# Kernel tuning notes

Hardware: AMD Instinct MI355X
Metric: run time of the kernel (lower is better)

The kernel has to match this reference:

```python
import jax, jax.numpy as jnp
import numpy as np

# fixed geometry: N = B2D * H * W pixels
B2D, H, W = 32, 112, 112
NCLS, NSUB, DIM = 4, 2, 256
PROTO_MOM = 0.999
SK_ITERS, SK_EPS = 3, 0.05
LN_EPS = 1e-5


def layer_norm(x, gamma, beta):
    mu = jnp.mean(x, axis=-1, keepdims=True)
    var = jnp.var(x, axis=-1, keepdims=True)
    return (x - mu) * jax.lax.rsqrt(var + LN_EPS) * gamma + beta


def l2_normalize(x):
    return x / jnp.maximum(jnp.linalg.norm(x, axis=-1, keepdims=True), 1e-12)


def masked_sinkhorn(sim_c, mask):
    # sim_c: [N, M] cosine sims for one class; mask: [N] bool (pixels of this class)
    # Faithful to distributed_sinkhorn, restricted to masked rows.
    m = mask.astype(sim_c.dtype)
    L = jnp.exp(sim_c / SK_EPS).T * m[None, :]          # [M, N]
    Bn = jnp.sum(m)
    M = L.shape[0]
    L = L / jnp.maximum(jnp.sum(L), 1e-30)
    for _ in range(SK_ITERS):
        L = L / jnp.maximum(jnp.sum(L, axis=1, keepdims=True), 1e-30) / M
        col = jnp.sum(L, axis=0, keepdims=True)
        L = jnp.where(m[None, :] > 0, L / jnp.maximum(col, 1e-30) / jnp.maximum(Bn, 1.0), 0.0)
    L = (L * Bn).T                                       # [N, M]
    idx = jnp.argmax(L, axis=1)
    q = jax.nn.one_hot(idx, M, dtype=sim_c.dtype) * m[:, None]  # hard assignment
    return q, idx


def setup_inputs() -> dict:
    key = jax.random.key(0)
    ks = jax.random.split(key, 3)
    N = B2D * H * W
    return {
        "out_feat": jax.random.normal(ks[0], (N, DIM), dtype=jnp.float32),
        "label": jax.random.randint(ks[1], (N,), 0, NCLS, dtype=jnp.int64),
        "prototypes": jax.random.normal(ks[2], (NCLS, NSUB, DIM), dtype=jnp.float32),
        "fn_gamma": jnp.ones((DIM,), jnp.float32),
        "fn_beta": jnp.zeros((DIM,), jnp.float32),
        "mn_gamma": jnp.ones((NCLS,), jnp.float32),
        "mn_beta": jnp.zeros((NCLS,), jnp.float32),
    }


def reference(out_feat, label, prototypes, fn_gamma, fn_beta, mn_gamma, mn_beta):
    N = out_feat.shape[0]
    feat = l2_normalize(layer_norm(out_feat, fn_gamma, fn_beta))      # [N, D]
    protos = l2_normalize(prototypes)                                  # [K, M, D]
    sim = jnp.einsum('nd,kmd->nmk', feat, protos)                      # [N, M, K]
    nearest = layer_norm(jnp.max(sim, axis=1), mn_gamma, mn_beta)      # [N, K]
    pred = jnp.argmax(nearest, axis=-1)
    correct = (label == pred)                                          # [N] bool

    proto_logits = sim.reshape(N, NSUB * NCLS)
    proto_target = jnp.zeros((N,), jnp.float32)
    new_protos = protos
    for c in range(NCLS):
        cls_mask = (label == c)
        q, idx = masked_sinkhorn(sim[:, :, c], cls_mask)               # q:[N,M], masked
        mk = (cls_mask & correct).astype(feat.dtype)[:, None]
        m_q = q * mk                                                   # [N, M]
        f = m_q.T @ (feat * mk)                                        # [M, D]
        n = jnp.sum(m_q, axis=0)                                       # [M]
        f = l2_normalize(f)
        upd = PROTO_MOM * protos[c] + (1.0 - PROTO_MOM) * f
        upd = jnp.where(((jnp.sum(n) > 0) & (n != 0))[:, None], upd, protos[c])
        new_protos = new_protos.at[c].set(upd)
        proto_target = jnp.where(cls_mask, idx.astype(jnp.float32) + NSUB * c, proto_target)
    new_protos = l2_normalize(new_protos)

    nearest_img = nearest.reshape(B2D, H, W, NCLS).transpose(0, 3, 1, 2)  # [b, K, h, w]
    return nearest_img, proto_logits, proto_target, new_protos
```

## Files before the change

kernel.cpp:

```cpp
#include <hip/hip_runtime.h>
#include <stdint.h>

#define N_PIX 401408
#define HWIMG 12544
#define LN_EPS 1e-5f

struct Ws {
  double R[3][8];
  unsigned cnt4[4];
  unsigned nmk[8];
  float  protoN[8][256];
  float  fAcc[8][256];
  unsigned char flags[N_PIX];
};

__device__ __forceinline__ float wredf(float v) {
#pragma unroll
  for (int o = 32; o > 0; o >>= 1) v += __shfl_xor(v, o, 64);
  return v;
}
__device__ __forceinline__ float wred16(float v) {
  v += __shfl_xor(v, 1, 64);
  v += __shfl_xor(v, 2, 64);
  v += __shfl_xor(v, 4, 64);
  v += __shfl_xor(v, 8, 64);
  return v;
}
__device__ __forceinline__ double wredd(double v) {
#pragma unroll
  for (int o = 32; o > 0; o >>= 1) v += __shfl_xor(v, o, 64);
  return v;
}
__device__ __forceinline__ unsigned wredu(unsigned v) {
#pragma unroll
  for (int o = 32; o > 0; o >>= 1) v += (unsigned)__shfl_xor((int)v, o, 64);
  return v;
}

__global__ __launch_bounds__(256) void k_main(
    const float* __restrict__ X, const int* __restrict__ label,
    const float* __restrict__ protos,
    const float* __restrict__ fng, const float* __restrict__ fnb,
    const float* __restrict__ mng, const float* __restrict__ mnb,
    Ws* __restrict__ ws,
    float* __restrict__ out_nearest, float* __restrict__ out_logits) {
  __shared__ float prS[16 * 132];
  int tid = threadIdx.x;
  int wave = tid >> 6, lane = tid & 63;

  if (blockIdx.x == 0) {
    if (tid < 24) ((double*)ws->R)[tid] = 0.0;
    if (tid >= 24 && tid < 32) ws->nmk[tid - 24] = 0u;
    if (tid >= 32 && tid < 36) ws->cnt4[tid - 32] = 0u;
    for (int i = tid; i < 2048; i += 256) (&ws->fAcc[0][0])[i] = 0.f;
  }

#pragma unroll
  for (int t = 0; t < 2; t++) {
    int r = wave + t * 4;
    const float4 p = *(const float4*)(protos + r * 256 + lane * 4);
    float ss = p.x * p.x + p.y * p.y + p.z * p.z + p.w * p.w;
    ss = wredf(ss);
    float inv = 1.0f / fmaxf(sqrtf(ss), 1e-12f);
    float4 o; o.x = p.x * inv; o.y = p.y * inv; o.z = p.z * inv; o.w = p.w * inv;
    int sd = lane >> 2;
    *(float4*)(&prS[sd * 132 + r * 16 + (lane & 3) * 4]) = o;
    if (blockIdx.x == 0) *(float4*)(&ws->protoN[r][lane * 4]) = o;
  }
  __syncthreads();

  int grp = lane >> 4, s = lane & 15;
  int n = blockIdx.x * 16 + wave * 4 + grp;

  const float* xb = X + (size_t)n * 256 + s * 16;
  const float4 x0 = *(const float4*)(xb);
  const float4 x1 = *(const float4*)(xb + 4);
  const float4 x2 = *(const float4*)(xb + 8);
  const float4 x3 = *(const float4*)(xb + 12);
  int lab = label[n];

  float sm = (x0.x + x0.y + x0.z + x0.w) + (x1.x + x1.y + x1.z + x1.w) +
             (x2.x + x2.y + x2.z + x2.w) + (x3.x + x3.y + x3.z + x3.w);
  float q = x0.x * x0.x + x0.y * x0.y + x0.z * x0.z + x0.w * x0.w +
            x1.x * x1.x + x1.y * x1.y + x1.z * x1.z + x1.w * x1.w +
            x2.x * x2.x + x2.y * x2.y + x2.z * x2.z + x2.w * x2.w +
            x3.x * x3.x + x3.y * x3.y + x3.z * x3.z + x3.w * x3.w;
  sm = wred16(sm); q = wred16(q);
  float mu = sm * (1.0f / 256.0f);
  float var = q * (1.0f / 256.0f) - mu * mu;
  float rstd = rsqrtf(var + LN_EPS);

  const float* gb = fng + s * 16;
  const float* bb = fnb + s * 16;
  const float4 g0 = *(const float4*)(gb);
  const float4 g1 = *(const float4*)(gb + 4);
  const float4 g2 = *(const float4*)(gb + 8);
  const float4 g3 = *(const float4*)(gb + 12);
  const float4 b0 = *(const float4*)(bb);
  const float4 b1 = *(const float4*)(bb + 4);
  const float4 b2 = *(const float4*)(bb + 8);
  const float4 b3 = *(const float4*)(bb + 12);

  float4 y0, y1, y2, y3;
  y0.x = (x0.x - mu) * rstd * g0.x + b0.x; y0.y = (x0.y - mu) * rstd * g0.y + b0.y;
  y0.z = (x0.z - mu) * rstd * g0.z + b0.z; y0.w = (x0.w - mu) * rstd * g0.w + b0.w;
  y1.x = (x1.x - mu) * rstd * g1.x + b1.x; y1.y = (x1.y - mu) * rstd * g1.y + b1.y;
  y1.z = (x1.z - mu) * rstd * g1.z + b1.z; y1.w = (x1.w - mu) * rstd * g1.w + b1.w;
  y2.x = (x2.x - mu) * rstd * g2.x + b2.x; y2.y = (x2.y - mu) * rstd * g2.y + b2.y;
  y2.z = (x2.z - mu) * rstd * g2.z + b2.z; y2.w = (x2.w - mu) * rstd * g2.w + b2.w;
  y3.x = (x3.x - mu) * rstd * g3.x + b3.x; y3.y = (x3.y - mu) * rstd * g3.y + b3.y;
  y3.z = (x3.z - mu) * rstd * g3.z + b3.z; y3.w = (x3.w - mu) * rstd * g3.w + b3.w;

  float qq = y0.x * y0.x + y0.y * y0.y + y0.z * y0.z + y0.w * y0.w +
             y1.x * y1.x + y1.y * y1.y + y1.z * y1.z + y1.w * y1.w +
             y2.x * y2.x + y2.y * y2.y + y2.z * y2.z + y2.w * y2.w +
             y3.x * y3.x + y3.y * y3.y + y3.z * y3.z + y3.w * y3.w;
  qq = wred16(qq);

  float dot[8];
#pragma unroll
  for (int j = 0; j < 8; j++) {
    const float* pj = &prS[s * 132 + j * 16];
    const float4 pa = *(const float4*)(pj);
    const float4 pb = *(const float4*)(pj + 4);
    const float4 pc = *(const float4*)(pj + 8);
    const float4 pd = *(const float4*)(pj + 12);
    dot[j] = y0.x * pa.x + y0.y * pa.y + y0.z * pa.z + y0.w * pa.w +
             y1.x * pb.x + y1.y * pb.y + y1.z * pb.z + y1.w * pb.w +
             y2.x * pc.x + y2.y * pc.y + y2.z * pc.z + y2.w * pc.w +
             y3.x * pd.x + y3.y * pd.y + y3.z * pd.z + y3.w * pd.w;
  }
#pragma unroll
  for (int o = 1; o <= 4; o <<= 1) {
#pragma unroll
    for (int j = 0; j < 8; j++) dot[j] += __shfl_xor(dot[j], o, 64);
  }
  int bsel = s & 7;
  float t0 = (bsel & 1) ? dot[1] : dot[0];
  float t1 = (bsel & 1) ? dot[3] : dot[2];
  float t2 = (bsel & 1) ? dot[5] : dot[4];
  float t3 = (bsel & 1) ? dot[7] : dot[6];
  float u0 = (bsel & 2) ? t1 : t0;
  float u1v = (bsel & 2) ? t3 : t2;
  float v = (bsel & 4) ? u1v : u0;
  v += __shfl_xor(v, 8, 64);

  float inv = 1.0f / fmaxf(sqrtf(qq), 1e-12f);
  float d = v * inv;

  if (s < 8) out_logits[(size_t)n * 8 + ((s & 1) << 2) + (s >> 1)] = d;

  float nm = fmaxf(d, __shfl_xor(d, 1, 64));
  float tA = __shfl_xor(nm, 2, 64);
  float s2 = nm + tA, q2 = nm * nm + tA * tA;
  float s4 = s2 + __shfl_xor(s2, 4, 64);
  float q4 = q2 + __shfl_xor(q2, 4, 64);
  float m4 = 0.25f * s4;
  float v4 = 0.25f * q4 - m4 * m4;
  float rs4 = rsqrtf(v4 + LN_EPS);
  int k = (s >> 1) & 3;
  float lnv = (nm - m4) * rs4 * mng[k] + mnb[k];

  int bimg = n / HWIMG;
  int p = n - bimg * HWIMG;
  if (s < 8 && (s & 1) == 0)
    out_nearest[((size_t)bimg * 4 + k) * HWIMG + p] = lnv;

  float av = lnv; int ak = k;
#pragma unroll
  for (int o = 2; o <= 4; o <<= 1) {
    float ov = __shfl_xor(av, o, 64);
    int ok = __shfl_xor(ak, o, 64);
    bool take = (ov > av) || (ov == av && ok < ak);
    av = take ? ov : av;
    ak = take ? ok : ak;
  }
  if (s == 0) ws->flags[n] = (lab == ak) ? (unsigned char)1 : (unsigned char)0;
}

template <int ITER>
__global__ __launch_bounds__(256) void k_sink(const float* __restrict__ logits,
                                              const int* __restrict__ label,
                                              Ws* __restrict__ ws) {
  __shared__ float su1[8], su2[8], sBn[4];
  int tid = threadIdx.x;
  if (ITER >= 2) {
    if (tid < 8) {
      int c = tid >> 1;
      float S = (float)ws->R[0][c * 2] + (float)ws->R[0][c * 2 + 1];
      float uu0 = 1.0f / fmaxf(S, 1e-30f);
      float R0 = (float)ws->R[0][tid];
      float uu1 = uu0 / (fmaxf(uu0 * R0, 1e-30f) * 2.0f);
      su1[tid] = uu1;
      if (ITER >= 3) {
        float R1 = (float)ws->R[1][tid];
        su2[tid] = uu1 / (fmaxf(uu1 * R1, 1e-30f) * 2.0f);
      }
    }
    if (tid < 4) sBn[tid] = fmaxf((float)ws->cnt4[tid], 1.0f);
  }
  __syncthreads();

  double a0 = 0, a1 = 0, a2 = 0, a3 = 0, a4 = 0, a5 = 0, a6 = 0, a7 = 0;
  unsigned c0 = 0, c1 = 0, c2 = 0, c3 = 0;
  int gtid = blockIdx.x * 256 + tid;
  int T = gridDim.x * 256;
  for (int n = gtid; n < N_PIX; n += T) {
    int c = label[n];
    const float4 la = *(const float4*)(logits + (size_t)n * 8);
    const float4 lb = *(const float4*)(logits + (size_t)n * 8 + 4);
    float s0 = (c & 2) ? ((c & 1) ? la.w : la.z) : ((c & 1) ? la.y : la.x);
    float s1 = (c & 2) ? ((c & 1) ? lb.w : lb.z) : ((c & 1) ? lb.y : lb.x);
    float E0 = expf(s0 / 0.05f);
    float E1 = expf(s1 / 0.05f);
    float v = 1.0f;
    if (ITER >= 2) {
      float S1 = su1[c * 2] * E0 + su1[c * 2 + 1] * E1;
      float v1 = 1.0f / (fmaxf(S1, 1e-30f) * sBn[c]);
      v = v1;
      if (ITER >= 3) {
        float S2 = su2[c * 2] * E0 + su2[c * 2 + 1] * E1;
        v = v1 / (fmaxf(v1 * S2, 1e-30f) * sBn[c]);
      }
    }
    double t0 = (double)(v * E0), t1 = (double)(v * E1);
    if (c == 0) { a0 += t0; a1 += t1; c0++; }
    else if (c == 1) { a2 += t0; a3 += t1; c1++; }
    else if (c == 2) { a4 += t0; a5 += t1; c2++; }
    else { a6 += t0; a7 += t1; c3++; }
  }
  a0 = wredd(a0); a1 = wredd(a1); a2 = wredd(a2); a3 = wredd(a3);
  a4 = wredd(a4); a5 = wredd(a5); a6 = wredd(a6); a7 = wredd(a7);
  __shared__ double lds[4][8];
  __shared__ unsigned ldc[4][4];
  int wave = tid >> 6, lane = tid & 63;
  if (ITER == 1) { c0 = wredu(c0); c1 = wredu(c1); c2 = wredu(c2); c3 = wredu(c3); }
  if (lane == 0) {
    lds[wave][0] = a0; lds[wave][1] = a1; lds[wave][2] = a2; lds[wave][3] = a3;
    lds[wave][4] = a4; lds[wave][5] = a5; lds[wave][6] = a6; lds[wave][7] = a7;
    if (ITER == 1) { ldc[wave][0] = c0; ldc[wave][1] = c1; ldc[wave][2] = c2; ldc[wave][3] = c3; }
  }
  __syncthreads();
  if (tid < 8) {
    double ssum = lds[0][tid] + lds[1][tid] + lds[2][tid] + lds[3][tid];
    unsafeAtomicAdd(&ws->R[ITER - 1][tid], ssum);
  }
  if (ITER == 1 && tid < 4) {
    unsigned cs = ldc[0][tid] + ldc[1][tid] + ldc[2][tid] + ldc[3][tid];
    atomicAdd(&ws->cnt4[tid], cs);
  }
}

__global__ __launch_bounds__(256) void k_accum(
    const float* __restrict__ X, const int* __restrict__ label,
    const float* __restrict__ fng, const float* __restrict__ fnb,
    const float* __restrict__ logits, Ws* __restrict__ ws,
    float* __restrict__ out_target) {
  __shared__ float fa[4 * 2048];
  __shared__ float su[8];
  __shared__ unsigned ldc[4][8];
  int tid = threadIdx.x;
  if (tid < 8) {
    int c = tid >> 1;
    float S = (float)ws->R[0][c * 2] + (float)ws->R[0][c * 2 + 1];
    float uu0 = 1.0f / fmaxf(S, 1e-30f);
    float R0 = (float)ws->R[0][tid];
    float uu1 = uu0 / (fmaxf(uu0 * R0, 1e-30f) * 2.0f);
    float R1 = (float)ws->R[1][tid];
    float uu2 = uu1 / (fmaxf(uu1 * R1, 1e-30f) * 2.0f);
    float R2 = (float)ws->R[2][tid];
    su[tid] = uu2 / (fmaxf(uu2 * R2, 1e-30f) * 2.0f);
  }
  for (int i = tid; i < 4 * 2048; i += 256) fa[i] = 0.f;
  __syncthreads();

  int wave = tid >> 6, lane = tid & 63;
  const float4 g4 = *(const float4*)(fng + lane * 4);
  const float4 b4 = *(const float4*)(fnb + lane * 4);
  float* myAcc = &fa[wave * 2048];

  unsigned cl[8] = {0, 0, 0, 0, 0, 0, 0, 0};
  int gw = blockIdx.x * 4 + wave;
  int GW = gridDim.x * 4;
  for (int ch = gw; ch < N_PIX / 64; ch += GW) {
    int n = ch * 64 + lane;
    int c = label[n];
    int fl = ws->flags[n];
    float s0 = logits[(size_t)n * 8 + c];
    float s1 = logits[(size_t)n * 8 + 4 + c];
    float E0 = expf(s0 / 0.05f);
    float E1 = expf(s1 / 0.05f);
    int idx = (su[c * 2 + 1] * E1 > su[c * 2] * E0) ? 1 : 0;
    out_target[n] = (float)(idx + 2 * c);
    int bucket = c * 2 + idx;
#pragma unroll
    for (int j = 0; j < 8; j++) cl[j] += (fl && bucket == j) ? 1u : 0u;

    unsigned long long mask = __ballot(fl);
    while (mask) {
      int src = __builtin_ctzll(mask);
      mask &= (mask - 1);
      int cc = __shfl(c, src, 64);
      int ii = __shfl(idx, src, 64);
      int nn = ch * 64 + src;
      const float4 x = *(const float4*)(X + (size_t)nn * 256 + lane * 4);
      float s = x.x + x.y + x.z + x.w;
      float q = x.x * x.x + x.y * x.y + x.z * x.z + x.w * x.w;
      s = wredf(s); q = wredf(q);
      float mu = s * (1.0f / 256.0f);
      float var = q * (1.0f / 256.0f) - mu * mu;
      float rstd = rsqrtf(var + LN_EPS);
      float y0 = (x.x - mu) * rstd * g4.x + b4.x;
      float y1 = (x.y - mu) * rstd * g4.y + b4.y;
      float y2 = (x.z - mu) * rstd * g4.z + b4.z;
      float y3 = (x.w - mu) * rstd * g4.w + b4.w;
      float qq = y0 * y0 + y1 * y1 + y2 * y2 + y3 * y3;
      qq = wredf(qq);
      float inv = 1.0f / fmaxf(sqrtf(qq), 1e-12f);
      float* dst = myAcc + (cc * 2 + ii) * 256 + lane * 4;
      dst[0] += y0 * inv; dst[1] += y1 * inv; dst[2] += y2 * inv; dst[3] += y3 * inv;
    }
  }
#pragma unroll
  for (int j = 0; j < 8; j++) cl[j] = wredu(cl[j]);
  if (lane == 0) {
#pragma unroll
    for (int j = 0; j < 8; j++) ldc[wave][j] = cl[j];
  }
  __syncthreads();
  float* fg = &ws->fAcc[0][0];
  for (int i = tid; i < 2048; i += 256) {
    float ssum = fa[i] + fa[2048 + i] + fa[4096 + i] + fa[6144 + i];
    unsafeAtomicAdd(fg + i, ssum);
  }
  if (tid < 8) {
    unsigned cs = ldc[0][tid] + ldc[1][tid] + ldc[2][tid] + ldc[3][tid];
    if (cs) atomicAdd(&ws->nmk[tid], cs);
  }
}

__global__ __launch_bounds__(512) void k_final(Ws* __restrict__ ws, float* __restrict__ out_protos) {
  int tid = threadIdx.x;
  int r = tid >> 6, lane = tid & 63;
  const float4 f = *(const float4*)(&ws->fAcc[r][lane * 4]);
  float ss = wredf(f.x * f.x + f.y * f.y + f.z * f.z + f.w * f.w);
  float invf = 1.0f / fmaxf(sqrtf(ss), 1e-12f);
  unsigned nr = ws->nmk[r];
  int c = r >> 1;
  unsigned tot = ws->nmk[c * 2] + ws->nmk[c * 2 + 1];
  bool cond = (tot > 0u) && (nr != 0u);
  const float4 p = *(const float4*)(&ws->protoN[r][lane * 4]);
  float u0 = cond ? 0.999f * p.x + 0.001f * (f.x * invf) : p.x;
  float u1 = cond ? 0.999f * p.y + 0.001f * (f.y * invf) : p.y;
  float u2 = cond ? 0.999f * p.z + 0.001f * (f.z * invf) : p.z;
  float u3 = cond ? 0.999f * p.w + 0.001f * (f.w * invf) : p.w;
  float ss2 = wredf(u0 * u0 + u1 * u1 + u2 * u2 + u3 * u3);
  float invn = 1.0f / fmaxf(sqrtf(ss2), 1e-12f);
  float4 o; o.x = u0 * invn; o.y = u1 * invn; o.z = u2 * invn; o.w = u3 * invn;
  *(float4*)(out_protos + r * 256 + lane * 4) = o;
}

extern "C" void kernel_launch(void* const* d_in, const int* in_sizes, int n_in,
                              void* d_out, int out_size, void* d_ws, size_t ws_size,
                              hipStream_t stream) {
  const float* X = (const float*)d_in[0];
  const int* label = (const int*)d_in[1];
  const float* protos = (const float*)d_in[2];
  const float* fng = (const float*)d_in[3];
  const float* fnb = (const float*)d_in[4];
  const float* mng = (const float*)d_in[5];
  const float* mnb = (const float*)d_in[6];

  float* out = (float*)d_out;
  float* out_nearest = out;
  float* out_logits = out + 1605632;
  float* out_target = out_logits + 3211264;
  float* out_protos = out_target + N_PIX;
  Ws* ws = (Ws*)d_ws;

  k_main<<<N_PIX / 16, 256, 0, stream>>>(X, label, protos, fng, fnb, mng, mnb, ws, out_nearest, out_logits);
  k_sink<1><<<512, 256, 0, stream>>>(out_logits, label, ws);
  k_sink<2><<<512, 256, 0, stream>>>(out_logits, label, ws);
  k_sink<3><<<512, 256, 0, stream>>>(out_logits, label, ws);
  k_accum<<<512, 256, 0, stream>>>(X, label, fng, fnb, out_logits, ws, out_target);
  k_final<<<1, 512, 0, stream>>>(ws, out_protos);
}
```

Measured before the change: 668.5 us.

## Fuse first Sinkhorn pass into main kernel and compact correct-pixel list

Folds the first Sinkhorn iteration (row sums and class counts) into k_main, which now stores the per-pixel exp values for the labelled class. Later Sinkhorn passes and the accumulate kernel read these precomputed exps instead of re-reading logits and recomputing exp. k_main also builds a global compacted list of correctly predicted pixels, so accumulation loops over only those pixels, four at a time, rather than scanning flags. It also swizzles the prototype shared-memory layout, makes feature loads coalesced, and moves workspace zeroing into its own launch. The cost is a larger workspace, extra block-level atomics and syncs in k_main, and a non-deterministic order in the correct list, which changes floating-point summation order.

```diff
diff --git a/kernel.cpp b/kernel.cpp
--- a/kernel.cpp
+++ b/kernel.cpp
@@ -9,9 +9,12 @@
   double R[3][8];
   unsigned cnt4[4];
   unsigned nmk[8];
+  unsigned nCorr;
+  unsigned pad[3];
   float  protoN[8][256];
   float  fAcc[8][256];
-  unsigned char flags[N_PIX];
+  float2 E2[N_PIX];
+  int    corrList[N_PIX];
 };
 
 __device__ __forceinline__ float wredf(float v) {
@@ -31,10 +34,14 @@
   for (int o = 32; o > 0; o >>= 1) v += __shfl_xor(v, o, 64);
   return v;
 }
-__device__ __forceinline__ unsigned wredu(unsigned v) {
-#pragma unroll
-  for (int o = 32; o > 0; o >>= 1) v += (unsigned)__shfl_xor((int)v, o, 64);
-  return v;
+
+__global__ __launch_bounds__(256) void k_zero(Ws* __restrict__ ws) {
+  int tid = threadIdx.x;
+  if (tid < 24) ((double*)ws->R)[tid] = 0.0;
+  else if (tid < 32) ws->nmk[tid - 24] = 0u;
+  else if (tid < 36) ws->cnt4[tid - 32] = 0u;
+  else if (tid == 36) ws->nCorr = 0u;
+  for (int i = tid; i < 2048; i += 256) (&ws->fAcc[0][0])[i] = 0.f;
 }
 
 __global__ __launch_bounds__(256) void k_main(
@@ -44,16 +51,14 @@
     const float* __restrict__ mng, const float* __restrict__ mnb,
     Ws* __restrict__ ws,
     float* __restrict__ out_nearest, float* __restrict__ out_logits) {
-  __shared__ float prS[16 * 132];
+  __shared__ float prS[2048];
+  __shared__ float sR4[4][8];
+  __shared__ unsigned sC4[4][4];
+  __shared__ unsigned sCorr, sBase;
+  __shared__ int sList[16];
   int tid = threadIdx.x;
   int wave = tid >> 6, lane = tid & 63;
-
-  if (blockIdx.x == 0) {
-    if (tid < 24) ((double*)ws->R)[tid] = 0.0;
-    if (tid >= 24 && tid < 32) ws->nmk[tid - 24] = 0u;
-    if (tid >= 32 && tid < 36) ws->cnt4[tid - 32] = 0u;
-    for (int i = tid; i < 2048; i += 256) (&ws->fAcc[0][0])[i] = 0.f;
-  }
+  if (tid == 0) sCorr = 0u;
 
 #pragma unroll
   for (int t = 0; t < 2; t++) {
@@ -63,8 +68,7 @@
     ss = wredf(ss);
     float inv = 1.0f / fmaxf(sqrtf(ss), 1e-12f);
     float4 o; o.x = p.x * inv; o.y = p.y * inv; o.z = p.z * inv; o.w = p.w * inv;
-    int sd = lane >> 2;
-    *(float4*)(&prS[sd * 132 + r * 16 + (lane & 3) * 4]) = o;
+    *(float4*)(&prS[lane * 32 + 4 * (r ^ (lane & 7))]) = o;
     if (blockIdx.x == 0) *(float4*)(&ws->protoN[r][lane * 4]) = o;
   }
   __syncthreads();
@@ -72,11 +76,11 @@
   int grp = lane >> 4, s = lane & 15;
   int n = blockIdx.x * 16 + wave * 4 + grp;
 
-  const float* xb = X + (size_t)n * 256 + s * 16;
+  const float* xb = X + (size_t)n * 256 + s * 4;
   const float4 x0 = *(const float4*)(xb);
-  const float4 x1 = *(const float4*)(xb + 4);
-  const float4 x2 = *(const float4*)(xb + 8);
-  const float4 x3 = *(const float4*)(xb + 12);
+  const float4 x1 = *(const float4*)(xb + 64);
+  const float4 x2 = *(const float4*)(xb + 128);
+  const float4 x3 = *(const float4*)(xb + 192);
   int lab = label[n];
 
   float sm = (x0.x + x0.y + x0.z + x0.w) + (x1.x + x1.y + x1.z + x1.w) +
@@ -90,16 +94,16 @@
   float var = q * (1.0f / 256.0f) - mu * mu;
   float rstd = rsqrtf(var + LN_EPS);
 
-  const float* gb = fng + s * 16;
-  const float* bb = fnb + s * 16;
+  const float* gb = fng + s * 4;
+  const float* bb = fnb + s * 4;
   const float4 g0 = *(const float4*)(gb);
-  const float4 g1 = *(const float4*)(gb + 4);
-  const float4 g2 = *(const float4*)(gb + 8);
-  const float4 g3 = *(const float4*)(gb + 12);
+  const float4 g1 = *(const float4*)(gb + 64);
+  const float4 g2 = *(const float4*)(gb + 128);
+  const float4 g3 = *(const float4*)(gb + 192);
   const float4 b0 = *(const float4*)(bb);
-  const float4 b1 = *(const float4*)(bb + 4);
-  const float4 b2 = *(const float4*)(bb + 8);
-  const float4 b3 = *(const float4*)(bb + 12);
+  const float4 b1 = *(const float4*)(bb + 64);
+  const float4 b2 = *(const float4*)(bb + 128);
+  const float4 b3 = *(const float4*)(bb + 192);
 
   float4 y0, y1, y2, y3;
   y0.x = (x0.x - mu) * rstd * g0.x + b0.x; y0.y = (x0.y - mu) * rstd * g0.y + b0.y;
@@ -120,33 +124,35 @@
   float dot[8];
 #pragma unroll
   for (int j = 0; j < 8; j++) {
-    const float* pj = &prS[s * 132 + j * 16];
-    const float4 pa = *(const float4*)(pj);
-    const float4 pb = *(const float4*)(pj + 4);
-    const float4 pc = *(const float4*)(pj + 8);
-    const float4 pd = *(const float4*)(pj + 12);
+    int jx = 4 * (j ^ (s & 7));
+    const float4 pa = *(const float4*)(&prS[s * 32 + jx]);
+    const float4 pb = *(const float4*)(&prS[(16 + s) * 32 + jx]);
+    const float4 pc = *(const float4*)(&prS[(32 + s) * 32 + jx]);
+    const float4 pd = *(const float4*)(&prS[(48 + s) * 32 + jx]);
     dot[j] = y0.x * pa.x + y0.y * pa.y + y0.z * pa.z + y0.w * pa.w +
              y1.x * pb.x + y1.y * pb.y + y1.z * pb.z + y1.w * pb.w +
              y2.x * pc.x + y2.y * pc.y + y2.z * pc.z + y2.w * pc.w +
              y3.x * pd.x + y3.y * pd.y + y3.z * pd.z + y3.w * pd.w;
   }
-#pragma unroll
-  for (int o = 1; o <= 4; o <<= 1) {
-#pragma unroll
-    for (int j = 0; j < 8; j++) dot[j] += __shfl_xor(dot[j], o, 64);
-  }
-  int bsel = s & 7;
-  float t0 = (bsel & 1) ? dot[1] : dot[0];
-  float t1 = (bsel & 1) ? dot[3] : dot[2];
-  float t2 = (bsel & 1) ? dot[5] : dot[4];
-  float t3 = (bsel & 1) ? dot[7] : dot[6];
-  float u0 = (bsel & 2) ? t1 : t0;
-  float u1v = (bsel & 2) ? t3 : t2;
-  float v = (bsel & 4) ? u1v : u0;
-  v += __shfl_xor(v, 8, 64);
-
-  float inv = 1.0f / fmaxf(sqrtf(qq), 1e-12f);
-  float d = v * inv;
+  int b0s = s & 1, b1s = (s >> 1) & 1, b2s = (s >> 2) & 1;
+  float e0 = b0s ? dot[1] : dot[0], o0 = b0s ? dot[0] : dot[1];
+  float e1 = b0s ? dot[3] : dot[2], o1 = b0s ? dot[2] : dot[3];
+  float e2 = b0s ? dot[5] : dot[4], o2 = b0s ? dot[4] : dot[5];
+  float e3 = b0s ? dot[7] : dot[6], o3 = b0s ? dot[6] : dot[7];
+  e0 += __shfl_xor(o0, 1, 64);
+  e1 += __shfl_xor(o1, 1, 64);
+  e2 += __shfl_xor(o2, 1, 64);
+  e3 += __shfl_xor(o3, 1, 64);
+  float f0 = b1s ? e1 : e0, p0 = b1s ? e0 : e1;
+  float f1 = b1s ? e3 : e2, p1 = b1s ? e2 : e3;
+  f0 += __shfl_xor(p0, 2, 64);
+  f1 += __shfl_xor(p1, 2, 64);
+  float h = b2s ? f1 : f0, ph = b2s ? f0 : f1;
+  h += __shfl_xor(ph, 4, 64);
+  float v = h + __shfl_xor(h, 8, 64);
+
+  float invq = 1.0f / fmaxf(sqrtf(qq), 1e-12f);
+  float d = v * invq;
 
   if (s < 8) out_logits[(size_t)n * 8 + ((s & 1) << 2) + (s >> 1)] = d;
 
@@ -175,87 +181,95 @@
     av = take ? ov : av;
     ak = take ? ok : ak;
   }
-  if (s == 0) ws->flags[n] = (lab == ak) ? (unsigned char)1 : (unsigned char)0;
+
+  float Ev = expf(d / 0.05f);
+  bool isLab = (s < 8) && ((s >> 1) == lab);
+  if (isLab) ((float*)(ws->E2 + n))[s & 1] = Ev;
+  float val = isLab ? Ev : 0.f;
+  val += __shfl_xor(val, 16, 64);
+  val += __shfl_xor(val, 32, 64);
+  unsigned cu = ((s < 8) && !(s & 1) && ((s >> 1) == lab)) ? 1u : 0u;
+  cu += (unsigned)__shfl_xor((int)cu, 16, 64);
+  cu += (unsigned)__shfl_xor((int)cu, 32, 64);
+  if (lane < 8) sR4[wave][lane] = val;
+  if (lane < 8 && !(lane & 1)) sC4[wave][lane >> 1] = cu;
+
+  bool corr = (s == 0) && (lab == ak);
+  if (corr) { unsigned pos = atomicAdd(&sCorr, 1u); sList[pos] = n; }
+  __syncthreads();
+  if (tid == 0) sBase = atomicAdd(&ws->nCorr, sCorr);
+  if (tid < 8) {
+    double rs = (double)sR4[0][tid] + (double)sR4[1][tid] +
+                (double)sR4[2][tid] + (double)sR4[3][tid];
+    unsafeAtomicAdd(&ws->R[0][tid], rs);
+  }
+  if (tid < 4) {
+    unsigned cs = sC4[0][tid] + sC4[1][tid] + sC4[2][tid] + sC4[3][tid];
+    if (cs) atomicAdd(&ws->cnt4[tid], cs);
+  }
+  __syncthreads();
+  if (tid < sCorr) ws->corrList[sBase + tid] = sList[tid];
 }
 
 template <int ITER>
-__global__ __launch_bounds__(256) void k_sink(const float* __restrict__ logits,
-                                              const int* __restrict__ label,
+__global__ __launch_bounds__(256) void k_sink(const int* __restrict__ label,
                                               Ws* __restrict__ ws) {
   __shared__ float su1[8], su2[8], sBn[4];
   int tid = threadIdx.x;
-  if (ITER >= 2) {
-    if (tid < 8) {
-      int c = tid >> 1;
-      float S = (float)ws->R[0][c * 2] + (float)ws->R[0][c * 2 + 1];
-      float uu0 = 1.0f / fmaxf(S, 1e-30f);
-      float R0 = (float)ws->R[0][tid];
-      float uu1 = uu0 / (fmaxf(uu0 * R0, 1e-30f) * 2.0f);
-      su1[tid] = uu1;
-      if (ITER >= 3) {
-        float R1 = (float)ws->R[1][tid];
-        su2[tid] = uu1 / (fmaxf(uu1 * R1, 1e-30f) * 2.0f);
-      }
-    }
-    if (tid < 4) sBn[tid] = fmaxf((float)ws->cnt4[tid], 1.0f);
-  }
+  if (tid < 8) {
+    int c = tid >> 1;
+    float S = (float)ws->R[0][c * 2] + (float)ws->R[0][c * 2 + 1];
+    float uu0 = 1.0f / fmaxf(S, 1e-30f);
+    float R0 = (float)ws->R[0][tid];
+    float uu1 = uu0 / (fmaxf(uu0 * R0, 1e-30f) * 2.0f);
+    su1[tid] = uu1;
+    if (ITER >= 3) {
+      float R1 = (float)ws->R[1][tid];
+      su2[tid] = uu1 / (fmaxf(uu1 * R1, 1e-30f) * 2.0f);
+    }
+  }
+  if (tid < 4) sBn[tid] = fmaxf((float)ws->cnt4[tid], 1.0f);
   __syncthreads();
 
   double a0 = 0, a1 = 0, a2 = 0, a3 = 0, a4 = 0, a5 = 0, a6 = 0, a7 = 0;
-  unsigned c0 = 0, c1 = 0, c2 = 0, c3 = 0;
   int gtid = blockIdx.x * 256 + tid;
   int T = gridDim.x * 256;
   for (int n = gtid; n < N_PIX; n += T) {
     int c = label[n];
-    const float4 la = *(const float4*)(logits + (size_t)n * 8);
-    const float4 lb = *(const float4*)(logits + (size_t)n * 8 + 4);
-    float s0 = (c & 2) ? ((c & 1) ? la.w : la.z) : ((c & 1) ? la.y : la.x);
-    float s1 = (c & 2) ? ((c & 1) ? lb.w : lb.z) : ((c & 1) ? lb.y : lb.x);
-    float E0 = expf(s0 / 0.05f);
-    float E1 = expf(s1 / 0.05f);
-    float v = 1.0f;
-    if (ITER >= 2) {
-      float S1 = su1[c * 2] * E0 + su1[c * 2 + 1] * E1;
-      float v1 = 1.0f / (fmaxf(S1, 1e-30f) * sBn[c]);
-      v = v1;
-      if (ITER >= 3) {
-        float S2 = su2[c * 2] * E0 + su2[c * 2 + 1] * E1;
-        v = v1 / (fmaxf(v1 * S2, 1e-30f) * sBn[c]);
-      }
+    float2 e = ws->E2[n];
+    float E0 = e.x, E1 = e.y;
+    float S1 = su1[c * 2] * E0 + su1[c * 2 + 1] * E1;
+    float v1 = 1.0f / (fmaxf(S1, 1e-30f) * sBn[c]);
+    float v = v1;
+    if (ITER >= 3) {
+      float S2 = su2[c * 2] * E0 + su2[c * 2 + 1] * E1;
+      v = v1 / (fmaxf(v1 * S2, 1e-30f) * sBn[c]);
     }
     double t0 = (double)(v * E0), t1 = (double)(v * E1);
-    if (c == 0) { a0 += t0; a1 += t1; c0++; }
-    else if (c == 1) { a2 += t0; a3 += t1; c1++; }
-    else if (c == 2) { a4 += t0; a5 += t1; c2++; }
-    else { a6 += t0; a7 += t1; c3++; }
+    if (c == 0) { a0 += t0; a1 += t1; }
+    else if (c == 1) { a2 += t0; a3 += t1; }
+    else if (c == 2) { a4 += t0; a5 += t1; }
+    else { a6 += t0; a7 += t1; }
   }
   a0 = wredd(a0); a1 = wredd(a1); a2 = wredd(a2); a3 = wredd(a3);
   a4 = wredd(a4); a5 = wredd(a5); a6 = wredd(a6); a7 = wredd(a7);
   __shared__ double lds[4][8];
-  __shared__ unsigned ldc[4][4];
   int wave = tid >> 6, lane = tid & 63;
-  if (ITER == 1) { c0 = wredu(c0); c1 = wredu(c1); c2 = wredu(c2); c3 = wredu(c3); }
   if (lane == 0) {
     lds[wave][0] = a0; lds[wave][1] = a1; lds[wave][2] = a2; lds[wave][3] = a3;
     lds[wave][4] = a4; lds[wave][5] = a5; lds[wave][6] = a6; lds[wave][7] = a7;
-    if (ITER == 1) { ldc[wave][0] = c0; ldc[wave][1] = c1; ldc[wave][2] = c2; ldc[wave][3] = c3; }
   }
   __syncthreads();
   if (tid < 8) {
     double ssum = lds[0][tid] + lds[1][tid] + lds[2][tid] + lds[3][tid];
     unsafeAtomicAdd(&ws->R[ITER - 1][tid], ssum);
   }
-  if (ITER == 1 && tid < 4) {
-    unsigned cs = ldc[0][tid] + ldc[1][tid] + ldc[2][tid] + ldc[3][tid];
-    atomicAdd(&ws->cnt4[tid], cs);
-  }
 }
 
 __global__ __launch_bounds__(256) void k_accum(
     const float* __restrict__ X, const int* __restrict__ label,
     const float* __restrict__ fng, const float* __restrict__ fnb,
-    const float* __restrict__ logits, Ws* __restrict__ ws,
-    float* __restrict__ out_target) {
+    Ws* __restrict__ ws, float* __restrict__ out_target) {
   __shared__ float fa[4 * 2048];
   __shared__ float su[8];
   __shared__ unsigned ldc[4][8];
@@ -274,55 +288,68 @@
   for (int i = tid; i < 4 * 2048; i += 256) fa[i] = 0.f;
   __syncthreads();
 
+  int gtid = blockIdx.x * 256 + tid;
+  int T = gridDim.x * 256;
+  for (int n = gtid; n < N_PIX; n += T) {
+    int c = label[n];
+    float2 e = ws->E2[n];
+    int idx = (su[c * 2 + 1] * e.y > su[c * 2] * e.x) ? 1 : 0;
+    out_target[n] = (float)(idx + 2 * c);
+  }
+
   int wave = tid >> 6, lane = tid & 63;
   const float4 g4 = *(const float4*)(fng + lane * 4);
   const float4 b4 = *(const float4*)(fnb + lane * 4);
   float* myAcc = &fa[wave * 2048];
-
   unsigned cl[8] = {0, 0, 0, 0, 0, 0, 0, 0};
-  int gw = blockIdx.x * 4 + wave;
-  int GW = gridDim.x * 4;
-  for (int ch = gw; ch < N_PIX / 64; ch += GW) {
-    int n = ch * 64 + lane;
-    int c = label[n];
-    int fl = ws->flags[n];
-    float s0 = logits[(size_t)n * 8 + c];
-    float s1 = logits[(size_t)n * 8 + 4 + c];
-    float E0 = expf(s0 / 0.05f);
-    float E1 = expf(s1 / 0.05f);
-    int idx = (su[c * 2 + 1] * E1 > su[c * 2] * E0) ? 1 : 0;
-    out_target[n] = (float)(idx + 2 * c);
-    int bucket = c * 2 + idx;
-#pragma unroll
-    for (int j = 0; j < 8; j++) cl[j] += (fl && bucket == j) ? 1u : 0u;
-
-    unsigned long long mask = __ballot(fl);
-    while (mask) {
-      int src = __builtin_ctzll(mask);
-      mask &= (mask - 1);
-      int cc = __shfl(c, src, 64);
-      int ii = __shfl(idx, src, 64);
-      int nn = ch * 64 + src;
-      const float4 x = *(const float4*)(X + (size_t)nn * 256 + lane * 4);
-      float s = x.x + x.y + x.z + x.w;
-      float q = x.x * x.x + x.y * x.y + x.z * x.z + x.w * x.w;
-      s = wredf(s); q = wredf(q);
-      float mu = s * (1.0f / 256.0f);
-      float var = q * (1.0f / 256.0f) - mu * mu;
+  unsigned nc = ws->nCorr;
+  unsigned gw = blockIdx.x * 4 + wave;
+  unsigned GW = gridDim.x * 4;
+  for (unsigned base = gw * 4; base < nc; base += GW * 4) {
+    int m = (int)min(4u, nc - base);
+    int bk[4]; float4 xx[4];
+#pragma unroll
+    for (int g = 0; g < 4; g++) if (g < m) {
+      int n = ws->corrList[base + g];
+      int c = label[n];
+      float2 e = ws->E2[n];
+      int idx = (su[c * 2 + 1] * e.y > su[c * 2] * e.x) ? 1 : 0;
+      bk[g] = c * 2 + idx;
+      xx[g] = *(const float4*)(X + (size_t)n * 256 + lane * 4);
+    }
+    float svr[4], qvr[4];
+#pragma unroll
+    for (int g = 0; g < 4; g++) if (g < m) {
+      float4 x = xx[g];
+      float sv = x.x + x.y + x.z + x.w;
+      float qv = x.x * x.x + x.y * x.y + x.z * x.z + x.w * x.w;
+      svr[g] = wredf(sv); qvr[g] = wredf(qv);
+    }
+    float4 yy[4]; float qqr[4];
+#pragma unroll
+    for (int g = 0; g < 4; g++) if (g < m) {
+      float mu = svr[g] * (1.0f / 256.0f);
+      float var = qvr[g] * (1.0f / 256.0f) - mu * mu;
       float rstd = rsqrtf(var + LN_EPS);
-      float y0 = (x.x - mu) * rstd * g4.x + b4.x;
-      float y1 = (x.y - mu) * rstd * g4.y + b4.y;
-      float y2 = (x.z - mu) * rstd * g4.z + b4.z;
-      float y3 = (x.w - mu) * rstd * g4.w + b4.w;
-      float qq = y0 * y0 + y1 * y1 + y2 * y2 + y3 * y3;
-      qq = wredf(qq);
-      float inv = 1.0f / fmaxf(sqrtf(qq), 1e-12f);
-      float* dst = myAcc + (cc * 2 + ii) * 256 + lane * 4;
-      dst[0] += y0 * inv; dst[1] += y1 * inv; dst[2] += y2 * inv; dst[3] += y3 * inv;
-    }
-  }
-#pragma unroll
-  for (int j = 0; j < 8; j++) cl[j] = wredu(cl[j]);
+      float4 x = xx[g];
+      float4 y;
+      y.x = (x.x - mu) * rstd * g4.x + b4.x;
+      y.y = (x.y - mu) * rstd * g4.y + b4.y;
+      y.z = (x.z - mu) * rstd * g4.z + b4.z;
+      y.w = (x.w - mu) * rstd * g4.w + b4.w;
+      yy[g] = y;
+      qqr[g] = wredf(y.x * y.x + y.y * y.y + y.z * y.z + y.w * y.w);
+    }
+#pragma unroll
+    for (int g = 0; g < 4; g++) if (g < m) {
+      float invq = 1.0f / fmaxf(sqrtf(qqr[g]), 1e-12f);
+      float4 y = yy[g];
+      float* dst = myAcc + bk[g] * 256 + lane * 4;
+      dst[0] += y.x * invq; dst[1] += y.y * invq;
+      dst[2] += y.z * invq; dst[3] += y.w * invq;
+      if (lane == 0) cl[bk[g]]++;
+    }
+  }
   if (lane == 0) {
 #pragma unroll
     for (int j = 0; j < 8; j++) ldc[wave][j] = cl[j];
@@ -378,10 +405,10 @@
   float* out_protos = out_target + N_PIX;
   Ws* ws = (Ws*)d_ws;
 
+  k_zero<<<1, 256, 0, stream>>>(ws);
   k_main<<<N_PIX / 16, 256, 0, stream>>>(X, label, protos, fng, fnb, mng, mnb, ws, out_nearest, out_logits);
-  k_sink<1><<<512, 256, 0, stream>>>(out_logits, label, ws);
-  k_sink<2><<<512, 256, 0, stream>>>(out_logits, label, ws);
-  k_sink<3><<<512, 256, 0, stream>>>(out_logits, label, ws);
-  k_accum<<<512, 256, 0, stream>>>(X, label, fng, fnb, out_logits, ws, out_target);
+  k_sink<2><<<512, 256, 0, stream>>>(label, ws);
+  k_sink<3><<<512, 256, 0, stream>>>(label, ws);
+  k_accum<<<512, 256, 0, stream>>>(X, label, fng, fnb, ws, out_target);
   k_final<<<1, 512, 0, stream>>>(ws, out_protos);
 }
```

After: 1.120 ms. +67.5%, slower.
